# Kernel optimization log

Measured on AMD Instinct MI355X. Metric: run time of the kernel, lower is better.

## Reference

```python
import jax, jax.numpy as jnp
import numpy as np

N, D, HID = 16384, 1024, 4096
IN_DIM = 4 * D + 1
LN_EPS = 1e-5


def setup_inputs() -> dict:
    key = jax.random.key(0)
    ks = jax.random.split(key, 8)
    # xavier_uniform for bilinear: bound = sqrt(6/(d+d))
    bb = float(np.sqrt(6.0 / (D + D)))
    w1b = float(np.sqrt(1.0 / IN_DIM))  # torch Linear default init bound
    w2b = float(np.sqrt(1.0 / HID))
    return {
        "zA": jax.random.normal(ks[0], (N, D), dtype=jnp.float32),
        "zB": jax.random.normal(ks[1], (N, D), dtype=jnp.float32),
        "bilinear": jax.random.uniform(ks[2], (D, D), minval=-bb, maxval=bb, dtype=jnp.float32),
        "ln_g": jnp.ones((IN_DIM,), dtype=jnp.float32),
        "ln_b": jnp.zeros((IN_DIM,), dtype=jnp.float32),
        "W1": jax.random.uniform(ks[3], (IN_DIM, HID), minval=-w1b, maxval=w1b, dtype=jnp.float32),
        "b1": jax.random.uniform(ks[4], (HID,), minval=-w1b, maxval=w1b, dtype=jnp.float32),
        "W2": jax.random.uniform(ks[5], (HID, D), minval=-w2b, maxval=w2b, dtype=jnp.float32),
        "b2": jax.random.uniform(ks[6], (D,), minval=-w2b, maxval=w2b, dtype=jnp.float32),
    }


def reference(zA, zB, bilinear, ln_g, ln_b, W1, b1, W2, b2):
    had = zA * zB                                   # [N, D]
    diff = jnp.abs(zA - zB)                         # [N, D]
    # diag(zA @ W @ zB^T) == sum((zA @ W) * zB, -1)  -- O(N d^2) not O(N^2 d)
    s = jnp.sum((zA @ bilinear) * zB, axis=-1, keepdims=True)  # [N, 1]
    x = jnp.concatenate([zA, zB, had, diff, s], axis=1)        # [N, 4D+1]
    # LayerNorm over last dim
    mu = jnp.mean(x, axis=-1, keepdims=True)
    var = jnp.mean(jnp.square(x - mu), axis=-1, keepdims=True)
    x = (x - mu) * jax.lax.rsqrt(var + LN_EPS) * ln_g + ln_b
    # Linear -> GELU (exact/erf, torch default) -> Linear -> GELU; dropout off (eval)
    h = jax.nn.gelu(x @ W1 + b1, approximate=False)            # [N, HID]
    out = jax.nn.gelu(h @ W2 + b2, approximate=False)          # [N, D]
    return out
```

## Files before the change

### kernel.cpp

```cpp
#include <hip/hip_runtime.h>
#include <math.h>

#define NROWS 16384
#define DDIM  1024
#define HIDD  4096

typedef __bf16 bf16;
typedef bf16 bf16x8 __attribute__((ext_vector_type(8)));
typedef bf16 bf16x4 __attribute__((ext_vector_type(4)));
typedef float f32x4 __attribute__((ext_vector_type(4)));

__device__ __forceinline__ float gelu_erf(float x) {
  return 0.5f * x * (1.0f + erff(x * 0.70710678118654752f));
}

__device__ __forceinline__ void gld16(const bf16* g, bf16* l) {
  __builtin_amdgcn_global_load_lds(
      (const __attribute__((address_space(1))) void*)g,
      (__attribute__((address_space(3))) void*)l, 16, 0, 0);
}

__global__ __launch_bounds__(256) void cast_bf16_k(const float* __restrict__ in,
                                                   bf16* __restrict__ out) {
  size_t i = (size_t)blockIdx.x * blockDim.x + threadIdx.x;
  float4 v = ((const float4*)in)[i];
  bf16x4 o = {(bf16)v.x, (bf16)v.y, (bf16)v.z, (bf16)v.w};
  ((bf16x4*)out)[i] = o;
}

__global__ __launch_bounds__(256) void transpose_cast_k(const float* __restrict__ in,
                                                        bf16* __restrict__ out,
                                                        int R, int C) {
  __shared__ float tile[32][33];
  int bx = blockIdx.x * 32, by = blockIdx.y * 32;
  int tx = threadIdx.x, ty = threadIdx.y;
  #pragma unroll
  for (int i = ty; i < 32; i += 8)
    tile[i][tx] = in[(size_t)(by + i) * C + bx + tx];
  __syncthreads();
  #pragma unroll
  for (int i = ty; i < 32; i += 8)
    out[(size_t)(bx + i) * R + by + tx] = (bf16)tile[tx][i];
}

__global__ __launch_bounds__(256) void rowfuse_k(
    const float* __restrict__ zA, const float* __restrict__ zB,
    const bf16* __restrict__ t, const float* __restrict__ lng,
    const float* __restrict__ lnb, bf16* __restrict__ x,
    float* __restrict__ s_ln) {
  int row = blockIdx.x, tid = threadIdx.x;
  float4 a4 = ((const float4*)(zA + (size_t)row * DDIM))[tid];
  float4 b4 = ((const float4*)(zB + (size_t)row * DDIM))[tid];
  bf16x4 t4 = ((const bf16x4*)(t + (size_t)row * DDIM))[tid];
  float av[4] = {a4.x, a4.y, a4.z, a4.w};
  float bv[4] = {b4.x, b4.y, b4.z, b4.w};
  float hv[4], dv[4];
  float s1 = 0.f, s2 = 0.f, sd = 0.f;
  #pragma unroll
  for (int j = 0; j < 4; j++) {
    hv[j] = av[j] * bv[j];
    dv[j] = fabsf(av[j] - bv[j]);
    s1 += av[j] + bv[j] + hv[j] + dv[j];
    s2 += av[j]*av[j] + bv[j]*bv[j] + hv[j]*hv[j] + dv[j]*dv[j];
    sd += (float)t4[j] * bv[j];
  }
  #pragma unroll
  for (int off = 32; off > 0; off >>= 1) {
    s1 += __shfl_xor(s1, off, 64);
    s2 += __shfl_xor(s2, off, 64);
    sd += __shfl_xor(sd, off, 64);
  }
  __shared__ float red[3][4];
  int wave = tid >> 6;
  if ((tid & 63) == 0) { red[0][wave] = s1; red[1][wave] = s2; red[2][wave] = sd; }
  __syncthreads();
  s1 = red[0][0] + red[0][1] + red[0][2] + red[0][3];
  s2 = red[1][0] + red[1][1] + red[1][2] + red[1][3];
  float s = red[2][0] + red[2][1] + red[2][2] + red[2][3];
  const float inv = 1.0f / 4097.0f;
  float mu = (s1 + s) * inv;
  float var = (s2 + s * s) * inv - mu * mu;
  float rs = rsqrtf(var + 1e-5f);
  bf16* xr = x + (size_t)row * 4096;
  #define WRITE_SEG(si, vals)                                            \
  {                                                                      \
    float4 gg = ((const float4*)lng)[(si)*256 + tid];                    \
    float4 bb = ((const float4*)lnb)[(si)*256 + tid];                    \
    const float* gp = (const float*)&gg;                                 \
    const float* bp = (const float*)&bb;                                 \
    bf16x4 o;                                                            \
    _Pragma("unroll") for (int j = 0; j < 4; j++)                        \
        o[j] = (bf16)((vals[j] - mu) * rs * gp[j] + bp[j]);              \
    ((bf16x4*)xr)[(si)*256 + tid] = o;                                   \
  }
  WRITE_SEG(0, av)
  WRITE_SEG(1, bv)
  WRITE_SEG(2, hv)
  WRITE_SEG(3, dv)
  #undef WRITE_SEG
  if (tid == 0) s_ln[row] = (s - mu) * rs * lng[4096] + lnb[4096];
}

template <int EPI>
__global__ __launch_bounds__(256) void gemm_bt_k(
    const bf16* __restrict__ A, const bf16* __restrict__ B, int K, int Nout,
    void* __restrict__ Cout, const float* __restrict__ bias,
    const float* __restrict__ srow, const float* __restrict__ wlast) {
  __shared__ alignas(16) bf16 As[128 * 64];
  __shared__ alignas(16) bf16 Bs[128 * 64];
  const int tid = threadIdx.x;
  const int wave = tid >> 6, lane = tid & 63;
  const int wm = wave >> 1, wn = wave & 1;
  const int lrow = lane & 15, quad = lane >> 4;
  const size_t rowA0 = (size_t)blockIdx.y * 128;
  const size_t rowB0 = (size_t)blockIdx.x * 128;

  f32x4 acc[4][4] = {};

  const int lchunk = (tid & 7) ^ ((tid >> 3) & 7);
  const bf16* gA = A + (rowA0 + (tid >> 3)) * (size_t)K + lchunk * 8;
  const bf16* gB = B + (rowB0 + (tid >> 3)) * (size_t)K + lchunk * 8;

  for (int kb = 0; kb < K; kb += 64) {
    const bf16* pa = gA + kb;
    const bf16* pb = gB + kb;
    #pragma unroll
    for (int it = 0; it < 4; it++) {
      gld16(pa + (size_t)it * 32 * K, As + it * 2048 + wave * 512);
      gld16(pb + (size_t)it * 32 * K, Bs + it * 2048 + wave * 512);
    }
    __syncthreads();
    #pragma unroll
    for (int kk = 0; kk < 2; kk++) {
      const int cla = ((kk * 4 + quad) ^ (lrow & 7)) * 8;
      bf16x8 af[4], bfr[4];
      #pragma unroll
      for (int mi = 0; mi < 4; mi++)
        af[mi] = *(const bf16x8*)(As + (wm * 64 + mi * 16 + lrow) * 64 + cla);
      #pragma unroll
      for (int ni = 0; ni < 4; ni++)
        bfr[ni] = *(const bf16x8*)(Bs + (wn * 64 + ni * 16 + lrow) * 64 + cla);
      #pragma unroll
      for (int mi = 0; mi < 4; mi++)
        #pragma unroll
        for (int ni = 0; ni < 4; ni++)
          acc[mi][ni] = __builtin_amdgcn_mfma_f32_16x16x32_bf16(af[mi], bfr[ni], acc[mi][ni], 0, 0, 0);
    }
    __syncthreads();
  }

  const size_t ldc = (size_t)Nout;
  #pragma unroll
  for (int mi = 0; mi < 4; mi++) {
    size_t row = rowA0 + wm * 64 + mi * 16 + quad * 4;
    float srv[4];
    if (EPI == 1) {
      #pragma unroll
      for (int r = 0; r < 4; r++) srv[r] = srow[row + r];
    }
    #pragma unroll
    for (int ni = 0; ni < 4; ni++) {
      size_t col = rowB0 + wn * 64 + ni * 16 + lrow;
      float bvv = (EPI != 0) ? bias[col] : 0.0f;
      float wl = (EPI == 1) ? wlast[col] : 0.0f;
      #pragma unroll
      for (int r = 0; r < 4; r++) {
        float v = acc[mi][ni][r];
        if (EPI == 1) v += bvv + srv[r] * wl;
        if (EPI == 2) v += bvv;
        if (EPI != 0) v = gelu_erf(v);
        size_t idx = (row + r) * ldc + col;
        if (EPI == 2) ((float*)Cout)[idx] = v;
        else ((bf16*)Cout)[idx] = (bf16)v;
      }
    }
  }
}

extern "C" void kernel_launch(void* const* d_in, const int* in_sizes, int n_in,
                              void* d_out, int out_size, void* d_ws, size_t ws_size,
                              hipStream_t stream) {
  const float* zA  = (const float*)d_in[0];
  const float* zB  = (const float*)d_in[1];
  const float* bil = (const float*)d_in[2];
  const float* lng = (const float*)d_in[3];
  const float* lnb = (const float*)d_in[4];
  const float* W1  = (const float*)d_in[5];
  const float* b1  = (const float*)d_in[6];
  const float* W2  = (const float*)d_in[7];
  const float* b2  = (const float*)d_in[8];
  float* out = (float*)d_out;

  char* ws = (char*)d_ws;
  const size_t SZ_BILT = (size_t)DDIM * DDIM * 2;
  const size_t SZ_W1T  = (size_t)4096 * 4096 * 2;
  const size_t SZ_W2T  = (size_t)DDIM * HIDD * 2;
  const size_t PERSIST = SZ_BILT + SZ_W1T + SZ_W2T;

  int C = 0;
  for (int cand = NROWS; cand >= 512; cand >>= 1) {
    size_t need = PERSIST + (size_t)16384 * cand + (size_t)4 * cand + 1024;
    if (need <= ws_size) { C = cand; break; }
  }
  if (C == 0) return;

  bf16* bilT = (bf16*)ws;
  bf16* W1T  = (bf16*)(ws + SZ_BILT);
  bf16* W2T  = (bf16*)(ws + SZ_BILT + SZ_W1T);
  char* dyn  = ws + PERSIST;
  bf16*  r1    = (bf16*)dyn;
  bf16*  zA_bf = r1;
  bf16*  t_bf  = r1 + (size_t)C * 1024;
  bf16*  h_bf  = r1;
  bf16*  x_bf  = (bf16*)(dyn + (size_t)8192 * C);
  float* s_ln  = (float*)(dyn + (size_t)16384 * C);

  dim3 tb(32, 8);
  transpose_cast_k<<<dim3(DDIM / 32, DDIM / 32), tb, 0, stream>>>(bil, bilT, DDIM, DDIM);
  transpose_cast_k<<<dim3(HIDD / 32, 4096 / 32), tb, 0, stream>>>(W1, W1T, 4096, HIDD);
  transpose_cast_k<<<dim3(DDIM / 32, HIDD / 32), tb, 0, stream>>>(W2, W2T, HIDD, DDIM);

  for (int r0 = 0; r0 < NROWS; r0 += C) {
    const float* zAc = zA + (size_t)r0 * DDIM;
    const float* zBc = zB + (size_t)r0 * DDIM;

    cast_bf16_k<<<(C * DDIM / 4) / 256, 256, 0, stream>>>(zAc, zA_bf);

    gemm_bt_k<0><<<dim3(DDIM / 128, C / 128), 256, 0, stream>>>(
        zA_bf, bilT, DDIM, DDIM, t_bf, nullptr, nullptr, nullptr);

    rowfuse_k<<<C, 256, 0, stream>>>(zAc, zBc, t_bf, lng, lnb, x_bf, s_ln);

    gemm_bt_k<1><<<dim3(HIDD / 128, C / 128), 256, 0, stream>>>(
        x_bf, W1T, 4096, HIDD, h_bf, b1, s_ln, W1 + (size_t)4096 * HIDD);

    gemm_bt_k<2><<<dim3(DDIM / 128, C / 128), 256, 0, stream>>>(
        h_bf, W2T, 4096, DDIM, out + (size_t)r0 * DDIM, b2, nullptr, nullptr);
  }
}
```

Before: 1.098 ms.

## Use 256x256 tile GEMM with deeper LDS pipeline for first MLP layer

Replaces the 128x128-tile GEMM for the W1 layer (the largest matmul) with a dedicated 512-thread kernel computing 256x256 output tiles. It uses direct global-to-LDS loads, double-buffered half-K staging, swizzled LDS layout, and phased MFMA with s_setprio and barriers to overlap loads with compute. Larger tiles raise arithmetic intensity and cut global traffic. The cost is higher register and LDS pressure (128 KB LDS per block, 2 blocks per CU requested) and fewer blocks per chunk, which could hurt occupancy or tail balance.

```diff
diff --git a/kernel.cpp b/kernel.cpp
--- a/kernel.cpp
+++ b/kernel.cpp
@@ -177,6 +177,109 @@
   }
 }
 
+__global__ __launch_bounds__(512, 2) void gemm256_epi1_k(
+    const bf16* __restrict__ A, const bf16* __restrict__ B, int K, int Nout,
+    bf16* __restrict__ Cout, const float* __restrict__ bias,
+    const float* __restrict__ srow, const float* __restrict__ wlast) {
+  __shared__ alignas(16) bf16 As[2][2][8192];
+  __shared__ alignas(16) bf16 Bs[2][2][8192];
+  const int tid = threadIdx.x;
+  const int wave = tid >> 6, lane = tid & 63;
+  const int wm = wave >> 2, wn = wave & 3;
+  const int lrow = lane & 15, quad = lane >> 4;
+  const int cswz = ((quad ^ ((lrow >> 1) & 3)) << 3);
+  const size_t rowA0 = (size_t)blockIdx.y * 256;
+  const size_t rowB0 = (size_t)blockIdx.x * 256;
+  const int Kmask = K - 1;
+
+  const int sr = tid >> 2;
+  const int sq = (tid & 3) ^ ((sr >> 1) & 3);
+  const bf16* gA = A + (rowA0 + sr) * (size_t)K + sq * 8;
+  const bf16* gB = B + (rowB0 + sr) * (size_t)K + sq * 8;
+  const size_t rstep = 128 * (size_t)K;
+  const int wofs = wave * 512;
+
+  f32x4 acc[8][4] = {};
+
+#define STG_A(b, h, ko) { const bf16* s_ = gA + ((ko) & Kmask);          \
+    gld16(s_, &As[b][h][wofs]); gld16(s_ + rstep, &As[b][h][4096 + wofs]); }
+#define STG_B(b, h, ko) { const bf16* s_ = gB + ((ko) & Kmask);          \
+    gld16(s_, &Bs[b][h][wofs]); gld16(s_ + rstep, &Bs[b][h][4096 + wofs]); }
+
+  STG_A(0, 0, 0)  STG_B(0, 0, 0)
+  STG_A(0, 1, 32) STG_B(0, 1, 32)
+  STG_A(1, 0, 64) STG_B(1, 0, 64)
+  asm volatile("s_waitcnt vmcnt(4)" ::: "memory");
+  __builtin_amdgcn_s_barrier();
+
+  bf16x8 af[8], bfr[2];
+  const int arow = wm * 128 + lrow;
+  const int brow = wn * 64 + lrow;
+
+#define LD_A(b, h) { _Pragma("unroll") for (int mi = 0; mi < 8; mi++)    \
+    af[mi] = *(const bf16x8*)(&As[b][h][(arow + mi * 16) * 32 + cswz]); }
+#define LD_B(b, h, nlo) { _Pragma("unroll") for (int nj = 0; nj < 2; nj++) \
+    bfr[nj] = *(const bf16x8*)(&Bs[b][h][(brow + ((nlo) + nj) * 16) * 32 + cswz]); }
+#define MFMA_HALF(nlo) { _Pragma("unroll") for (int mi = 0; mi < 8; mi++) {           \
+    acc[mi][nlo] = __builtin_amdgcn_mfma_f32_16x16x32_bf16(af[mi], bfr[0], acc[mi][nlo], 0, 0, 0);       \
+    acc[mi][(nlo)+1] = __builtin_amdgcn_mfma_f32_16x16x32_bf16(af[mi], bfr[1], acc[mi][(nlo)+1], 0, 0, 0); } }
+#define PH(bufc, khc, nlo, LOADA, STAGE, VW) {                           \
+    if (LOADA) LD_A(bufc, khc)                                           \
+    LD_B(bufc, khc, nlo)                                                 \
+    STAGE                                                                \
+    __builtin_amdgcn_s_barrier();                                        \
+    asm volatile("s_waitcnt lgkmcnt(0)" ::: "memory");                   \
+    __builtin_amdgcn_s_setprio(1);                                       \
+    MFMA_HALF(nlo)                                                       \
+    __builtin_amdgcn_s_setprio(0);                                       \
+    VW                                                                   \
+    __builtin_amdgcn_s_barrier(); }
+
+  const int NI = K >> 7;
+  int kb = 0;
+  #pragma unroll 1
+  for (int i = 0; i < NI; ++i, kb += 128) {
+    PH(0, 0, 0, 1, STG_A(1, 1, kb + 96), )
+    PH(0, 0, 2, 0, STG_B(1, 1, kb + 96), )
+    PH(0, 1, 0, 1, STG_A(0, 0, kb + 128), )
+    PH(0, 1, 2, 0, STG_B(0, 0, kb + 128),
+       asm volatile("s_waitcnt vmcnt(4)" ::: "memory");)
+    PH(1, 0, 0, 1, STG_A(0, 1, kb + 160), )
+    PH(1, 0, 2, 0, STG_B(0, 1, kb + 160), )
+    PH(1, 1, 0, 1, STG_A(1, 0, kb + 192), )
+    PH(1, 1, 2, 0, STG_B(1, 0, kb + 192),
+       asm volatile("s_waitcnt vmcnt(4)" ::: "memory");)
+  }
+  asm volatile("s_waitcnt vmcnt(0)" ::: "memory");
+#undef PH
+#undef MFMA_HALF
+#undef LD_B
+#undef LD_A
+#undef STG_B
+#undef STG_A
+
+  const size_t ldc = (size_t)Nout;
+  #pragma unroll
+  for (int mi = 0; mi < 8; mi++) {
+    size_t row = rowA0 + wm * 128 + mi * 16 + quad * 4;
+    float srv[4];
+    #pragma unroll
+    for (int r = 0; r < 4; r++) srv[r] = srow[row + r];
+    #pragma unroll
+    for (int ni = 0; ni < 4; ni++) {
+      size_t col = rowB0 + wn * 64 + ni * 16 + lrow;
+      float bvv = bias[col];
+      float wl = wlast[col];
+      #pragma unroll
+      for (int r = 0; r < 4; r++) {
+        float v = acc[mi][ni][r] + bvv + srv[r] * wl;
+        v = gelu_erf(v);
+        Cout[(row + r) * ldc + col] = (bf16)v;
+      }
+    }
+  }
+}
+
 extern "C" void kernel_launch(void* const* d_in, const int* in_sizes, int n_in,
                               void* d_out, int out_size, void* d_ws, size_t ws_size,
                               hipStream_t stream) {
@@ -231,7 +334,7 @@
 
     rowfuse_k<<<C, 256, 0, stream>>>(zAc, zBc, t_bf, lng, lnb, x_bf, s_ln);
 
-    gemm_bt_k<1><<<dim3(HIDD / 128, C / 128), 256, 0, stream>>>(
+    gemm256_epi1_k<<<dim3(HIDD / 256, C / 256), 512, 0, stream>>>(
         x_bf, W1T, 4096, HIDD, h_bf, b1, s_ln, W1 + (size_t)4096 * HIDD);
 
     gemm_bt_k<2><<<dim3(DDIM / 128, C / 128), 256, 0, stream>>>(
```

Measured after the change: 1.061 ms. -3.3%, faster.
